# Kernel optimization log

Hardware: AMD Instinct MI355X
Metric: run time of the kernel (lower is better)

Reference implementation:

```python
import jax, jax.numpy as jnp
import numpy as np

D_MODEL = 1024
N_HEADS = 16
D_K = D_MODEL // N_HEADS
SEQ = 4096
BATCH = 2
THETA = 10000.0


def _rope(x, token_positions):
    # x: [b, h, s, d_k], token_positions: [s] int
    half = D_K // 2
    inv_freq = 1.0 / (THETA ** (jnp.arange(0, D_K, 2, dtype=jnp.float32) / D_K))  # [half]
    freqs = token_positions.astype(jnp.float32)[:, None] * inv_freq[None, :]      # [s, half]
    cos, sin = jnp.cos(freqs), jnp.sin(freqs)                                     # [s, half]
    xe = x[..., 0::2]
    xo = x[..., 1::2]
    out_e = xe * cos - xo * sin
    out_o = xe * sin + xo * cos
    # interleave even/odd back: [..., s, half, 2] -> [..., s, d_k]
    return jnp.stack([out_e, out_o], axis=-1).reshape(x.shape)


def setup_inputs() -> dict:
    key = jax.random.key(0)
    ks = jax.random.split(key, 5)
    std = (2.0 / (D_MODEL + D_MODEL)) ** 0.5
    x = jax.random.normal(ks[0], (BATCH, SEQ, D_MODEL), dtype=jnp.float32)
    Wq = jax.random.normal(ks[1], (D_MODEL, D_MODEL), dtype=jnp.float32) * std
    Wk = jax.random.normal(ks[2], (D_MODEL, D_MODEL), dtype=jnp.float32) * std
    Wv = jax.random.normal(ks[3], (D_MODEL, D_MODEL), dtype=jnp.float32) * std
    Wo = jax.random.normal(ks[4], (D_MODEL, D_MODEL), dtype=jnp.float32) * std
    token_positions = jnp.arange(SEQ, dtype=jnp.int32)
    return {"x": x, "token_positions": token_positions, "Wq": Wq, "Wk": Wk, "Wv": Wv, "Wo": Wo}


def reference(x, token_positions, Wq, Wk, Wv, Wo):
    B, S, _ = x.shape

    def proj(W):
        y = jnp.einsum('bsd,od->bso', x, W)                     # [b, s, d_model]
        return y.reshape(B, S, N_HEADS, D_K).transpose(0, 2, 1, 3)  # [b, h, s, d_k]

    q, k, v = proj(Wq), proj(Wk), proj(Wv)
    q = _rope(q, token_positions)
    k = _rope(k, token_positions)

    scale = 1.0 / np.sqrt(D_K).astype(np.float32)
    scores = jnp.einsum('bhqd,bhkd->bhqk', q, k) * scale        # [b, h, s, s]
    causal = jnp.tril(jnp.ones((S, S), dtype=bool))
    scores = jnp.where(causal[None, None], scores, -jnp.inf)
    probs = jax.nn.softmax(scores, axis=-1)
    out = jnp.einsum('bhqk,bhkd->bhqd', probs, v)               # [b, h, s, d_k]
    out = out.transpose(0, 2, 1, 3).reshape(B, S, D_MODEL)
    return jnp.einsum('bsd,od->bso', out, Wo)
```

## Files before the change

### kernel.cpp

```cpp
#include <hip/hip_runtime.h>
#include <hip/hip_bf16.h>

typedef unsigned short u16;
typedef __attribute__((ext_vector_type(4))) float f32x4;
typedef __attribute__((ext_vector_type(16))) float f32x16;
typedef __attribute__((ext_vector_type(8))) short s16x8;
typedef __attribute__((ext_vector_type(2))) unsigned u32x2;

constexpr int DMODEL = 1024;
constexpr int NH     = 16;
constexpr int DK     = 64;
constexpr int SEQ    = 4096;
constexpr int BATCH  = 2;
constexpr int BS     = BATCH * SEQ;
constexpr int NX     = BS * DMODEL;
constexpr int NW     = DMODEL * DMODEL;

__device__ __forceinline__ unsigned pk2(float a, float b) {
  float2 t; t.x = a; t.y = b;
  __hip_bfloat162 h = __float22bfloat162_rn(t);
  return *reinterpret_cast<unsigned*>(&h);
}
__device__ __forceinline__ float bf2f(u16 h) {
  union { unsigned u; float f; } v; v.u = ((unsigned)h) << 16;
  return v.f;
}
__device__ __forceinline__ u32x2 plswap(unsigned a, unsigned b) {
  return __builtin_amdgcn_permlane32_swap(a, b, false, false);
}
__device__ __forceinline__ f32x16 mfma32(s16x8 a, s16x8 b, f32x16 c) {
  return __builtin_amdgcn_mfma_f32_32x32x16_bf16(a, b, c, 0, 0, 0);
}
__device__ __forceinline__ void gload_lds16(const void* g, void* l) {
  __builtin_amdgcn_global_load_lds(
      (const __attribute__((address_space(1))) void*)g,
      (__attribute__((address_space(3))) void*)l, 16, 0, 0);
}
__device__ __forceinline__ float exp2raw(float x) {
  return __builtin_amdgcn_exp2f(x);
}

__global__ __launch_bounds__(256) void convert_all(
    const float* __restrict__ x, const float* __restrict__ wq,
    const float* __restrict__ wk, const float* __restrict__ wv,
    const float* __restrict__ wo, u16* __restrict__ xb, u16* __restrict__ Wb) {
  int t = blockIdx.x * 256 + threadIdx.x;
  int i = t * 4;
  const float* src; u16* dst;
  if (i < NX) { src = x + i; dst = xb + i; }
  else {
    int j = i - NX; int w = j >> 20; int jj = j & (NW - 1);
    src = (w == 0 ? wq : w == 1 ? wk : w == 2 ? wv : wo) + jj;
    dst = Wb + j;
  }
  float4 v = *reinterpret_cast<const float4*>(src);
  uint2 pk; pk.x = pk2(v.x, v.y); pk.y = pk2(v.z, v.w);
  *reinterpret_cast<uint2*>(dst) = pk;
}

template <int EPI>
__global__ __launch_bounds__(256) void gemm128(
    const u16* __restrict__ A, const u16* __restrict__ B,
    u16* __restrict__ Qw, u16* __restrict__ Kw, u16* __restrict__ Vt,
    float* __restrict__ Co) {
  __shared__ u16 lA[128 * 32];
  __shared__ u16 lB[128 * 32];
  const int tid = threadIdx.x, w = tid >> 6, l = tid & 63;
  const int wr = w >> 1, wc = w & 1;
  const int m0 = blockIdx.y * 128, n0 = blockIdx.x * 128;
  constexpr int K = 1024;
  f32x4 acc[4][4] = {};
  const int li = l & 15, lg = l >> 4;
  const int srow = l >> 2, skc = (l & 3) * 8;
  for (int k0 = 0; k0 < K; k0 += 32) {
    __syncthreads();
#pragma unroll
    for (int cc = 0; cc < 2; ++cc) {
      const int c = 2 * w + cc;
      const int row = c * 16 + srow;
      gload_lds16(A + (size_t)(m0 + row) * K + k0 + skc, &lA[c * 512]);
      gload_lds16(B + (size_t)(n0 + row) * K + k0 + skc, &lB[c * 512]);
    }
    __syncthreads();
    s16x8 af[4], bfr[4];
#pragma unroll
    for (int i = 0; i < 4; ++i)
      af[i] = *reinterpret_cast<const s16x8*>(&lA[(wr * 64 + i * 16 + li) * 32 + lg * 8]);
#pragma unroll
    for (int j = 0; j < 4; ++j)
      bfr[j] = *reinterpret_cast<const s16x8*>(&lB[(wc * 64 + j * 16 + li) * 32 + lg * 8]);
#pragma unroll
    for (int i = 0; i < 4; ++i)
#pragma unroll
      for (int j = 0; j < 4; ++j) {
        if (EPI == 1)
          acc[i][j] = __builtin_amdgcn_mfma_f32_16x16x32_bf16(af[i], bfr[j], acc[i][j], 0, 0, 0);
        else
          acc[i][j] = __builtin_amdgcn_mfma_f32_16x16x32_bf16(bfr[j], af[i], acc[i][j], 0, 0, 0);
      }
  }
#pragma unroll
  for (int i = 0; i < 4; ++i) {
#pragma unroll
    for (int j = 0; j < 4; ++j) {
      if (EPI == 0) {
        const int m = m0 + wr * 64 + i * 16 + li;
        const int b = m >> 12, s = m & (SEQ - 1);
        const int n = n0 + wc * 64 + j * 16 + lg * 4;
        const int which = n >> 10, nn = n & 1023, h = nn >> 6, d0 = nn & 63;
        u16* dst = (which == 0 ? Qw : Kw) + ((size_t)(b * NH + h) * SEQ + s) * DK + d0;
        uint2 pk;
        pk.x = pk2(acc[i][j][0], acc[i][j][1]);
        pk.y = pk2(acc[i][j][2], acc[i][j][3]);
        *reinterpret_cast<uint2*>(dst) = pk;
      } else if (EPI == 1) {
        const int mbase = m0 + wr * 64 + i * 16 + lg * 4;
        const int b = mbase >> 12, s0 = mbase & (SEQ - 1);
        const int n = n0 + wc * 64 + j * 16 + li;
        const int h = n >> 6, d = n & 63;
        u16* dst = Vt + ((size_t)(b * NH + h) * DK + d) * SEQ + s0;
        uint2 pk;
        pk.x = pk2(acc[i][j][0], acc[i][j][1]);
        pk.y = pk2(acc[i][j][2], acc[i][j][3]);
        *reinterpret_cast<uint2*>(dst) = pk;
      } else {
        const int m = m0 + wr * 64 + i * 16 + li;
        const int n = n0 + wc * 64 + j * 16 + lg * 4;
        float4 v;
        v.x = acc[i][j][0]; v.y = acc[i][j][1]; v.z = acc[i][j][2]; v.w = acc[i][j][3];
        *reinterpret_cast<float4*>(&Co[(size_t)m * DMODEL + n]) = v;
      }
    }
  }
}

__global__ __launch_bounds__(256) void rope_qk(u16* __restrict__ Qw, u16* __restrict__ Kw,
                                               const int* __restrict__ pos) {
  const int TOT = BATCH * NH * SEQ * 32;
  int t = blockIdx.x * 256 + threadIdx.x;
  const bool isQ = (t < TOT);
  u16* arr = isQ ? Qw : Kw;
  int p = isQ ? t : t - TOT;
  const int i = p & 31;
  const int s = (p >> 5) & (SEQ - 1);
  const int bh = p >> 17;
  const float inv = expf(-(float)i * 0.28782313662425574f);
  const float ang = (float)pos[s] * inv;
  float sn, cs;
  sincosf(ang, &sn, &cs);
  const float sc = isQ ? 0.18033688011112042f : 1.0f;
  u16* ptr = arr + ((size_t)bh * SEQ + s) * DK + 2 * i;
  unsigned v = *reinterpret_cast<unsigned*>(ptr);
  float xe = bf2f((u16)(v & 0xffffu)), xo = bf2f((u16)(v >> 16));
  float oe = (xe * cs - xo * sn) * sc;
  float oo = (xe * sn + xo * cs) * sc;
  *reinterpret_cast<unsigned*>(ptr) = pk2(oe, oo);
}

__global__ __launch_bounds__(256, 2) void attn_kernel(
    const u16* __restrict__ Qw, const u16* __restrict__ Kw,
    const u16* __restrict__ Vt, u16* __restrict__ Ob) {
  __shared__ __align__(16) u16 Kb[2][8192];
  __shared__ __align__(16) u16 Vb[2][8192];
  const int tid = threadIdx.x, w = tid >> 6, l = tid & 63;
  const int lq = l & 31, hi = l >> 5;
  const int id = blockIdx.x;
  const int g = (id & 7) * 64 + (id >> 3);
  const int bh = g >> 4;
  const int j  = g & 15;
  const int tA = 31 - j, tB = j;
  const int nA = 32 - j;
  const int ntot = 33;
  const u16* Qh = Qw + (size_t)bh * SEQ * DK;
  const u16* Kh = Kw + (size_t)bh * SEQ * DK;
  const u16* Vh = Vt + (size_t)bh * DK * SEQ;
  const int b = bh >> 4, h = bh & 15;

  const s16x8 ones = {(short)0x3F80, (short)0x3F80, (short)0x3F80, (short)0x3F80,
                      (short)0x3F80, (short)0x3F80, (short)0x3F80, (short)0x3F80};

  s16x8 aq[4];
  f32x16 o0, o1, ls;

  auto loadQ = [&](int q0) {
#pragma unroll
    for (int ds = 0; ds < 4; ++ds)
      aq[ds] = *reinterpret_cast<const s16x8*>(
          &Qh[(size_t)(q0 + lq) * DK + ds * 16 + hi * 8]);
  };
  auto resetState = [&]() { o0 = f32x16{}; o1 = f32x16{}; ls = f32x16{}; };
  auto writeO = [&](int q0) {
    const float inv = 1.f / ls[0];
    u16* orow = Ob + ((size_t)(b * SEQ + q0 + lq)) * DMODEL + h * DK;
#pragma unroll
    for (int m = 0; m < 4; ++m) {
      uint2 pa;
      pa.x = pk2(o0[4 * m + 0] * inv, o0[4 * m + 1] * inv);
      pa.y = pk2(o0[4 * m + 2] * inv, o0[4 * m + 3] * inv);
      *reinterpret_cast<uint2*>(orow + 8 * m + 4 * hi) = pa;
      uint2 pb;
      pb.x = pk2(o1[4 * m + 0] * inv, o1[4 * m + 1] * inv);
      pb.y = pk2(o1[4 * m + 2] * inv, o1[4 * m + 3] * inv);
      *reinterpret_cast<uint2*>(orow + 32 + 8 * m + 4 * hi) = pb;
    }
  };
  auto stage = [&](int buf, int kt) {
    const int krow = tid >> 3;
    const int kcol = ((tid & 7) * 16) ^ ((krow & 7) << 4);
#pragma unroll
    for (int i = 0; i < 4; ++i)
      gload_lds16((const char*)Kh + (size_t)(kt + i * 32 + krow) * 128 + kcol,
                  (char*)&Kb[buf][0] + i * 4096 + tid * 16);
    const int vrow = tid >> 4;
    const int vcol = ((tid & 15) * 16) ^ ((vrow & 7) << 4);
#pragma unroll
    for (int i = 0; i < 4; ++i)
      gload_lds16((const char*)Vh + (size_t)(i * 16 + vrow) * (SEQ * 2) + kt * 2 + vcol,
                  (char*)&Vb[buf][0] + i * 4096 + tid * 16);
  };

  int q0 = tA * 128 + w * 32;
  loadQ(q0);
  resetState();
  stage(0, 0);
  int kt = 0;
  for (int it = 0; it < ntot; ++it) {
    asm volatile("s_waitcnt vmcnt(0)" ::: "memory");
    __builtin_amdgcn_s_barrier();
    __builtin_amdgcn_sched_barrier(0);
    const int itn = it + 1;
    const int ktn = (itn < nA) ? 128 * itn : (itn < ntot ? 128 * (itn - nA) : 0);
    stage(itn & 1, ktn);
    const int cur = it & 1;
#pragma unroll
    for (int sub = 0; sub < 2; ++sub) {
      const int ksub = kt + sub * 64;
      if (ksub > q0 + 31) continue;
      f32x16 s0 = {}, s1 = {};
      const char* kb = (const char*)&Kb[cur][0] + (sub * 64 + lq) * 128;
      __builtin_amdgcn_s_setprio(1);
#pragma unroll
      for (int ds = 0; ds < 4; ++ds) {
        const int co = (ds * 32 + hi * 16) ^ ((lq & 7) << 4);
        s16x8 k0 = *reinterpret_cast<const s16x8*>(kb + co);
        s16x8 k1 = *reinterpret_cast<const s16x8*>(kb + 32 * 128 + co);
        s0 = mfma32(k0, aq[ds], s0);
        s1 = mfma32(k1, aq[ds], s1);
      }
      __builtin_amdgcn_s_setprio(0);
      if (ksub + 63 > q0) {
#pragma unroll
        for (int r = 0; r < 16; ++r) {
          const int kr = (r & 3) + 8 * (r >> 2) + 4 * hi;
          if (ksub + kr > q0 + lq) s0[r] = -1e30f;
          if (ksub + 32 + kr > q0 + lq) s1[r] = -1e30f;
        }
      }
#pragma unroll
      for (int r = 0; r < 16; ++r) s0[r] = exp2raw(s0[r]);
#pragma unroll
      for (int r = 0; r < 16; ++r) s1[r] = exp2raw(s1[r]);
      unsigned U0[8], U1[8];
#pragma unroll
      for (int m = 0; m < 4; ++m) {
        U0[m * 2 + 0] = pk2(s0[4 * m + 0], s0[4 * m + 1]);
        U0[m * 2 + 1] = pk2(s0[4 * m + 2], s0[4 * m + 3]);
        U1[m * 2 + 0] = pk2(s1[4 * m + 0], s1[4 * m + 1]);
        U1[m * 2 + 1] = pk2(s1[4 * m + 2], s1[4 * m + 3]);
      }
      const char* vb = (const char*)&Vb[cur][0];
#pragma unroll
      for (int c16 = 0; c16 < 4; ++c16) {
        unsigned* U = (c16 < 2) ? U0 : U1;
        const int m0i = (c16 & 1) * 2, m1i = m0i + 1;
        u32x2 r0 = plswap(U[m0i * 2 + 0], U[m1i * 2 + 0]);
        u32x2 r1 = plswap(U[m0i * 2 + 1], U[m1i * 2 + 1]);
        union { uint4 u; s16x8 s; } cf;
        cf.u.x = r0.x; cf.u.y = r1.x; cf.u.z = r0.y; cf.u.w = r1.y;
        const int co = (sub * 128 + c16 * 32 + hi * 16) ^ ((lq & 7) << 4);
        s16x8 v0 = *reinterpret_cast<const s16x8*>(vb + lq * 256 + co);
        s16x8 v1 = *reinterpret_cast<const s16x8*>(vb + (32 + lq) * 256 + co);
        __builtin_amdgcn_s_setprio(1);
        o0 = mfma32(v0, cf.s, o0);
        o1 = mfma32(v1, cf.s, o1);
        ls = mfma32(ones, cf.s, ls);
        __builtin_amdgcn_s_setprio(0);
      }
    }
    if (it == nA - 1) {
      writeO(q0);
      q0 = tB * 128 + w * 32;
      loadQ(q0);
      resetState();
    }
    kt = ktn;
  }
  writeO(q0);
}

extern "C" void kernel_launch(void* const* d_in, const int* in_sizes, int n_in,
                              void* d_out, int out_size, void* d_ws, size_t ws_size,
                              hipStream_t stream) {
  const float* x  = (const float*)d_in[0];
  const int*  pos = (const int*)d_in[1];
  const float* wq = (const float*)d_in[2];
  const float* wk = (const float*)d_in[3];
  const float* wv = (const float*)d_in[4];
  const float* wo = (const float*)d_in[5];
  float* out = (float*)d_out;

  u16* Wb = (u16*)d_ws;
  u16* xb = Wb + 4 * (size_t)NW;
  u16* Qw = xb + (size_t)NX;
  u16* Kw = Qw + (size_t)NX;
  u16* Vt = Kw + (size_t)NX;
  u16* Ab = xb;

  convert_all<<<(NX + 4 * NW) / 4 / 256, 256, 0, stream>>>(x, wq, wk, wv, wo, xb, Wb);
  gemm128<0><<<dim3(16, 64), 256, 0, stream>>>(xb, Wb, Qw, Kw, nullptr, nullptr);
  gemm128<1><<<dim3(8, 64), 256, 0, stream>>>(xb, Wb + 2 * (size_t)NW, nullptr, nullptr, Vt, nullptr);
  rope_qk<<<2 * (BATCH * NH * SEQ * 32) / 256, 256, 0, stream>>>(Qw, Kw, pos);
  attn_kernel<<<512, 256, 0, stream>>>(Qw, Kw, Vt, Ab);
  gemm128<2><<<dim3(8, 64), 256, 0, stream>>>(Ab, Wb + 3 * (size_t)NW, nullptr, nullptr, nullptr, out);
}
```

Before: 249.6 us.

## Fuse RoPE into QK projection epilogue and split K/V staging in attention

Drops the standalone rope_qk kernel. A cos/sin table is precomputed inside the convert kernel, and the rotation plus Q scaling are applied in the QK GEMM epilogue before the bf16 store. The attention loop now stages K and V separately with partial vmcnt waits and an extra barrier, so the V load overlaps the QK^T/exp phase. P fragments are held in registers across the two phases. This removes a full read-modify-write pass over Q and K, at the cost of more register pressure and an extra barrier per iteration.

```diff
diff --git a/kernel.cpp b/kernel.cpp
--- a/kernel.cpp
+++ b/kernel.cpp
@@ -15,16 +15,13 @@
 constexpr int BS     = BATCH * SEQ;
 constexpr int NX     = BS * DMODEL;
 constexpr int NW     = DMODEL * DMODEL;
+constexpr float QSC  = 0.18033688011112042f;
 
 __device__ __forceinline__ unsigned pk2(float a, float b) {
   float2 t; t.x = a; t.y = b;
   __hip_bfloat162 h = __float22bfloat162_rn(t);
   return *reinterpret_cast<unsigned*>(&h);
 }
-__device__ __forceinline__ float bf2f(u16 h) {
-  union { unsigned u; float f; } v; v.u = ((unsigned)h) << 16;
-  return v.f;
-}
 __device__ __forceinline__ u32x2 plswap(unsigned a, unsigned b) {
   return __builtin_amdgcn_permlane32_swap(a, b, false, false);
 }
@@ -40,10 +37,22 @@
   return __builtin_amdgcn_exp2f(x);
 }
 
+constexpr int NTCONV = (NX + 4 * NW) / 4 / 256;
 __global__ __launch_bounds__(256) void convert_all(
     const float* __restrict__ x, const float* __restrict__ wq,
     const float* __restrict__ wk, const float* __restrict__ wv,
-    const float* __restrict__ wo, u16* __restrict__ xb, u16* __restrict__ Wb) {
+    const float* __restrict__ wo, u16* __restrict__ xb, u16* __restrict__ Wb,
+    const int* __restrict__ pos, float2* __restrict__ tab) {
+  if (blockIdx.x >= NTCONV) {
+    int t = (blockIdx.x - NTCONV) * 256 + threadIdx.x;
+    const int s = t >> 5, i = t & 31;
+    const float inv = expf(-(float)i * 0.28782313662425574f);
+    const float ang = (float)pos[s] * inv;
+    float sn, cs;
+    sincosf(ang, &sn, &cs);
+    tab[t] = make_float2(cs, sn);
+    return;
+  }
   int t = blockIdx.x * 256 + threadIdx.x;
   int i = t * 4;
   const float* src; u16* dst;
@@ -62,7 +71,7 @@
 __global__ __launch_bounds__(256) void gemm128(
     const u16* __restrict__ A, const u16* __restrict__ B,
     u16* __restrict__ Qw, u16* __restrict__ Kw, u16* __restrict__ Vt,
-    float* __restrict__ Co) {
+    float* __restrict__ Co, const float2* __restrict__ tab) {
   __shared__ u16 lA[128 * 32];
   __shared__ u16 lB[128 * 32];
   const int tid = threadIdx.x, w = tid >> 6, l = tid & 63;
@@ -105,13 +114,19 @@
     for (int j = 0; j < 4; ++j) {
       if (EPI == 0) {
         const int m = m0 + wr * 64 + i * 16 + li;
-        const int b = m >> 12, s = m & (SEQ - 1);
+        const int bb = m >> 12, s = m & (SEQ - 1);
         const int n = n0 + wc * 64 + j * 16 + lg * 4;
         const int which = n >> 10, nn = n & 1023, h = nn >> 6, d0 = nn & 63;
-        u16* dst = (which == 0 ? Qw : Kw) + ((size_t)(b * NH + h) * SEQ + s) * DK + d0;
-        uint2 pk;
-        pk.x = pk2(acc[i][j][0], acc[i][j][1]);
-        pk.y = pk2(acc[i][j][2], acc[i][j][3]);
+        const int i0 = d0 >> 1;
+        const float2 cs0 = tab[s * 32 + i0];
+        const float2 cs1 = tab[s * 32 + i0 + 1];
+        float oe0 = acc[i][j][0] * cs0.x - acc[i][j][1] * cs0.y;
+        float oo0 = acc[i][j][0] * cs0.y + acc[i][j][1] * cs0.x;
+        float oe1 = acc[i][j][2] * cs1.x - acc[i][j][3] * cs1.y;
+        float oo1 = acc[i][j][2] * cs1.y + acc[i][j][3] * cs1.x;
+        if (which == 0) { oe0 *= QSC; oo0 *= QSC; oe1 *= QSC; oo1 *= QSC; }
+        u16* dst = (which == 0 ? Qw : Kw) + ((size_t)(bb * NH + h) * SEQ + s) * DK + d0;
+        uint2 pk; pk.x = pk2(oe0, oo0); pk.y = pk2(oe1, oo1);
         *reinterpret_cast<uint2*>(dst) = pk;
       } else if (EPI == 1) {
         const int mbase = m0 + wr * 64 + i * 16 + lg * 4;
@@ -132,29 +147,6 @@
       }
     }
   }
-}
-
-__global__ __launch_bounds__(256) void rope_qk(u16* __restrict__ Qw, u16* __restrict__ Kw,
-                                               const int* __restrict__ pos) {
-  const int TOT = BATCH * NH * SEQ * 32;
-  int t = blockIdx.x * 256 + threadIdx.x;
-  const bool isQ = (t < TOT);
-  u16* arr = isQ ? Qw : Kw;
-  int p = isQ ? t : t - TOT;
-  const int i = p & 31;
-  const int s = (p >> 5) & (SEQ - 1);
-  const int bh = p >> 17;
-  const float inv = expf(-(float)i * 0.28782313662425574f);
-  const float ang = (float)pos[s] * inv;
-  float sn, cs;
-  sincosf(ang, &sn, &cs);
-  const float sc = isQ ? 0.18033688011112042f : 1.0f;
-  u16* ptr = arr + ((size_t)bh * SEQ + s) * DK + 2 * i;
-  unsigned v = *reinterpret_cast<unsigned*>(ptr);
-  float xe = bf2f((u16)(v & 0xffffu)), xo = bf2f((u16)(v >> 16));
-  float oe = (xe * cs - xo * sn) * sc;
-  float oo = (xe * sn + xo * cs) * sc;
-  *reinterpret_cast<unsigned*>(ptr) = pk2(oe, oo);
 }
 
 __global__ __launch_bounds__(256, 2) void attn_kernel(
@@ -204,13 +196,15 @@
       *reinterpret_cast<uint2*>(orow + 32 + 8 * m + 4 * hi) = pb;
     }
   };
-  auto stage = [&](int buf, int kt) {
+  auto stageK = [&](int buf, int kt) {
     const int krow = tid >> 3;
     const int kcol = ((tid & 7) * 16) ^ ((krow & 7) << 4);
 #pragma unroll
     for (int i = 0; i < 4; ++i)
       gload_lds16((const char*)Kh + (size_t)(kt + i * 32 + krow) * 128 + kcol,
                   (char*)&Kb[buf][0] + i * 4096 + tid * 16);
+  };
+  auto stageV = [&](int buf, int kt) {
     const int vrow = tid >> 4;
     const int vcol = ((tid & 15) * 16) ^ ((vrow & 7) << 4);
 #pragma unroll
@@ -222,20 +216,24 @@
   int q0 = tA * 128 + w * 32;
   loadQ(q0);
   resetState();
-  stage(0, 0);
+  stageK(0, 0);
+  stageV(0, 0);
   int kt = 0;
   for (int it = 0; it < ntot; ++it) {
-    asm volatile("s_waitcnt vmcnt(0)" ::: "memory");
+    asm volatile("s_waitcnt vmcnt(4)" ::: "memory");
     __builtin_amdgcn_s_barrier();
     __builtin_amdgcn_sched_barrier(0);
     const int itn = it + 1;
     const int ktn = (itn < nA) ? 128 * itn : (itn < ntot ? 128 * (itn - nA) : 0);
-    stage(itn & 1, ktn);
+    stageK(itn & 1, ktn);
     const int cur = it & 1;
+    s16x8 p[2][4];
+    const bool live0 = (kt <= q0 + 31);
+    const bool live1 = (kt + 64 <= q0 + 31);
 #pragma unroll
     for (int sub = 0; sub < 2; ++sub) {
+      if (!(sub == 0 ? live0 : live1)) continue;
       const int ksub = kt + sub * 64;
-      if (ksub > q0 + 31) continue;
       f32x16 s0 = {}, s1 = {};
       const char* kb = (const char*)&Kb[cur][0] + (sub * 64 + lq) * 128;
       __builtin_amdgcn_s_setprio(1);
@@ -268,7 +266,6 @@
         U1[m * 2 + 0] = pk2(s1[4 * m + 0], s1[4 * m + 1]);
         U1[m * 2 + 1] = pk2(s1[4 * m + 2], s1[4 * m + 3]);
       }
-      const char* vb = (const char*)&Vb[cur][0];
 #pragma unroll
       for (int c16 = 0; c16 < 4; ++c16) {
         unsigned* U = (c16 < 2) ? U0 : U1;
@@ -277,15 +274,28 @@
         u32x2 r1 = plswap(U[m0i * 2 + 1], U[m1i * 2 + 1]);
         union { uint4 u; s16x8 s; } cf;
         cf.u.x = r0.x; cf.u.y = r1.x; cf.u.z = r0.y; cf.u.w = r1.y;
+        p[sub][c16] = cf.s;
+      }
+    }
+    asm volatile("s_waitcnt vmcnt(4)" ::: "memory");
+    __builtin_amdgcn_s_barrier();
+    __builtin_amdgcn_sched_barrier(0);
+    stageV(itn & 1, ktn);
+    const char* vb = (const char*)&Vb[cur][0];
+#pragma unroll
+    for (int sub = 0; sub < 2; ++sub) {
+      if (!(sub == 0 ? live0 : live1)) continue;
+      __builtin_amdgcn_s_setprio(1);
+#pragma unroll
+      for (int c16 = 0; c16 < 4; ++c16) {
         const int co = (sub * 128 + c16 * 32 + hi * 16) ^ ((lq & 7) << 4);
         s16x8 v0 = *reinterpret_cast<const s16x8*>(vb + lq * 256 + co);
         s16x8 v1 = *reinterpret_cast<const s16x8*>(vb + (32 + lq) * 256 + co);
-        __builtin_amdgcn_s_setprio(1);
-        o0 = mfma32(v0, cf.s, o0);
-        o1 = mfma32(v1, cf.s, o1);
-        ls = mfma32(ones, cf.s, ls);
-        __builtin_amdgcn_s_setprio(0);
-      }
+        o0 = mfma32(v0, p[sub][c16], o0);
+        o1 = mfma32(v1, p[sub][c16], o1);
+        ls = mfma32(ones, p[sub][c16], ls);
+      }
+      __builtin_amdgcn_s_setprio(0);
     }
     if (it == nA - 1) {
       writeO(q0);
@@ -314,12 +324,12 @@
   u16* Qw = xb + (size_t)NX;
   u16* Kw = Qw + (size_t)NX;
   u16* Vt = Kw + (size_t)NX;
+  float2* tab = (float2*)(Vt + (size_t)NX);
   u16* Ab = xb;
 
-  convert_all<<<(NX + 4 * NW) / 4 / 256, 256, 0, stream>>>(x, wq, wk, wv, wo, xb, Wb);
-  gemm128<0><<<dim3(16, 64), 256, 0, stream>>>(xb, Wb, Qw, Kw, nullptr, nullptr);
-  gemm128<1><<<dim3(8, 64), 256, 0, stream>>>(xb, Wb + 2 * (size_t)NW, nullptr, nullptr, Vt, nullptr);
-  rope_qk<<<2 * (BATCH * NH * SEQ * 32) / 256, 256, 0, stream>>>(Qw, Kw, pos);
+  convert_all<<<NTCONV + 512, 256, 0, stream>>>(x, wq, wk, wv, wo, xb, Wb, pos, tab);
+  gemm128<0><<<dim3(16, 64), 256, 0, stream>>>(xb, Wb, Qw, Kw, nullptr, nullptr, tab);
+  gemm128<1><<<dim3(8, 64), 256, 0, stream>>>(xb, Wb + 2 * (size_t)NW, nullptr, nullptr, Vt, nullptr, nullptr);
   attn_kernel<<<512, 256, 0, stream>>>(Qw, Kw, Vt, Ab);
-  gemm128<2><<<dim3(8, 64), 256, 0, stream>>>(Ab, Wb + 3 * (size_t)NW, nullptr, nullptr, nullptr, out);
-}
+  gemm128<2><<<dim3(8, 64), 256, 0, stream>>>(Ab, Wb + 3 * (size_t)NW, nullptr, nullptr, nullptr, out, nullptr);
+}
```

Measured after the change: 236.0 us. -5.5%, faster.
